# Optimization experiments

Measured on AMD Instinct MI355X. Metric: run time of the kernel, lower is better.

Reference implementation:

```python
import jax, jax.numpy as jnp
import numpy as np

BS = 8192
NUM_CLASSES = 400
D = 768


def _bilin_from_14(m14, Y, X, eH, eW):
    # Value of bilinear-resize(m14 -> (eH,eW)) at integer pixel (Y,X), computed on the fly.
    # torch F.interpolate(align_corners=False): src = (dst+0.5)*in/out - 0.5, clamped at 0.
    # m14: (bs,14,14); Y,X: (bs,14) float integer-valued coords; eH,eW: (bs,) float.
    sy = jnp.maximum((Y + 0.5) * 14.0 / eH[:, None] - 0.5, 0.0)
    sx = jnp.maximum((X + 0.5) * 14.0 / eW[:, None] - 0.5, 0.0)
    r0f = jnp.floor(sy); c0f = jnp.floor(sx)
    r0 = r0f.astype(jnp.int32); r1 = jnp.minimum(r0 + 1, 13)
    c0 = c0f.astype(jnp.int32); c1 = jnp.minimum(c0 + 1, 13)
    fy = sy - r0f; fx = sx - c0f
    b = jnp.arange(m14.shape[0])[:, None, None]
    g00 = m14[b, r0[:, :, None], c0[:, None, :]]
    g01 = m14[b, r0[:, :, None], c1[:, None, :]]
    g10 = m14[b, r1[:, :, None], c0[:, None, :]]
    g11 = m14[b, r1[:, :, None], c1[:, None, :]]
    wy = fy[:, :, None]; wx = fx[:, None, :]
    return g00 * (1 - wy) * (1 - wx) + g01 * (1 - wy) * wx + g10 * wy * (1 - wx) + g11 * wy * wx


def _get_mask(attn, o_pos, e_pos):
    # Fused, fully-batched equivalent of the per-sample python loop:
    #   resize 14x14 -> (eH,eW) bilinear; crop (top,left,oH,oW); resize -> 14x14 bilinear.
    # The final resize only reads the intermediate grid at 4 integer points per output
    # pixel, so we evaluate those points lazily via _bilin_from_14 (exact, no Emax grid).
    bs = attn.shape[0]
    m14 = attn.reshape(bs, 14, 14)
    eH = e_pos[:, 2].astype(jnp.float32); eW = e_pos[:, 3].astype(jnp.float32)
    top = (o_pos[:, 0] - e_pos[:, 0]).astype(jnp.float32)
    left = (o_pos[:, 1] - e_pos[:, 1]).astype(jnp.float32)
    oH = o_pos[:, 2].astype(jnp.float32); oW = o_pos[:, 3].astype(jnp.float32)
    i = jnp.arange(14, dtype=jnp.float32)[None, :]
    ty = jnp.maximum((i + 0.5) * oH[:, None] / 14.0 - 0.5, 0.0)  # (bs,14) coords in crop
    tx = jnp.maximum((i + 0.5) * oW[:, None] / 14.0 - 0.5, 0.0)
    y0 = jnp.floor(ty); y1 = jnp.minimum(y0 + 1.0, oH[:, None] - 1.0); wy = ty - y0
    x0 = jnp.floor(tx); x1 = jnp.minimum(x0 + 1.0, oW[:, None] - 1.0); wx = tx - x0
    Y0 = top[:, None] + y0; Y1 = top[:, None] + y1  # absolute rows in (eH,eW) grid
    X0 = left[:, None] + x0; X1 = left[:, None] + x1
    v00 = _bilin_from_14(m14, Y0, X0, eH, eW)
    v01 = _bilin_from_14(m14, Y0, X1, eH, eW)
    v10 = _bilin_from_14(m14, Y1, X0, eH, eW)
    v11 = _bilin_from_14(m14, Y1, X1, eH, eW)
    wyc = wy[:, :, None]; wxc = wx[:, None, :]
    out = v00 * (1 - wyc) * (1 - wxc) + v01 * (1 - wyc) * wxc + v10 * wyc * (1 - wxc) + v11 * wyc * wxc
    return out.reshape(bs, 196)


def _get_att_mask(attention, ratio=0.5):
    bs = attention.shape[0]
    a14 = attention.reshape(bs, 14, 14)
    # bilinear 14->7 with align_corners=False samples at frac 0.5 == 2x2 average pool
    a7 = a14.reshape(bs, 7, 2, 7, 2).mean(axis=(2, 4))
    flat = a7.reshape(bs, 49)
    n_keep = int(49 * ratio) + 1  # argsort desc, take top N+1 = 25
    _, idx = jax.lax.top_k(flat, n_keep)
    masks = jnp.ones((bs, 49), dtype=bool)
    masks = masks.at[jnp.arange(bs)[:, None], idx].set(False)
    m7 = masks.reshape(bs, 7, 7)
    full = jnp.repeat(jnp.repeat(m7, 2, axis=1), 2, axis=2)
    return full.reshape(bs, 196)


def setup_inputs() -> dict:
    key = jax.random.key(0)
    k1, k2, k3 = jax.random.split(key, 3)
    attn = jax.random.uniform(k1, (BS, 196), dtype=jnp.float32)
    rng = np.random.default_rng(0)
    IMG = 224
    eH = rng.integers(112, IMG + 1, BS); eW = rng.integers(112, IMG + 1, BS)
    eT = rng.integers(0, IMG - eH + 1); eL = rng.integers(0, IMG - eW + 1)
    def box():
        h = rng.integers(56, eH + 1); w = rng.integers(56, eW + 1)
        t = eT + rng.integers(0, eH - h + 1); l = eL + rng.integers(0, eW - w + 1)
        return np.stack([t, l, h, w], axis=1)
    e = np.stack([eT, eL, eH, eW], axis=1)
    pos = np.stack([box(), box(), e], axis=1).astype(np.int32)  # (BS,3,4)
    image_embed = jax.random.normal(k2, (2 * BS, D), dtype=jnp.float32)
    W = jax.random.normal(k3, (NUM_CLASSES, D), dtype=jnp.float32) * 0.02
    b = jnp.zeros((NUM_CLASSES,), dtype=jnp.float32)
    return {"attn": attn, "pos": jnp.asarray(pos), "image_embed": image_embed, "W": W, "b": b}


def reference(attn, pos, image_embed, W, b):
    cm1 = _get_mask(attn, pos[:, 0], pos[:, 2])
    mask1 = _get_att_mask(cm1)
    cm2 = _get_mask(attn, pos[:, 1], pos[:, 2])
    mask2 = _get_att_mask(cm2)
    mask = jnp.concatenate([mask1, mask2], axis=0)  # (2*bs,196) bool, fed to masked encoder
    logits = image_embed @ W.T + b
    return logits, mask
```

## Files before the change

kernel.cpp:

```cpp
#include <hip/hip_runtime.h>
#include <hip/hip_bf16.h>
#include <stdint.h>
#include <type_traits>

#define BSAMP 8192
#define NCLS 400
#define DIM 768
#define LOGITS_SIZE (16384LL * 400LL)
#define GEMM_BLOCKS 640
#define MASK_BLOCKS 4096
#define W_ELEMS (NCLS * DIM)

typedef __attribute__((ext_vector_type(8))) short short8;
typedef __attribute__((ext_vector_type(4))) float floatx4;

__device__ inline unsigned int packbf(float a, float b) {
    unsigned int ua = __float_as_uint(a) + 0x8000u;
    unsigned int ub = __float_as_uint(b) + 0x8000u;
    return __builtin_amdgcn_perm(ub, ua, 0x07060302u);
}

__device__ inline short8 cvt8(float4 lo, float4 hi) {
    union { unsigned int u[4]; short8 s; } r;
    r.u[0] = packbf(lo.x, lo.y);
    r.u[1] = packbf(lo.z, lo.w);
    r.u[2] = packbf(hi.x, hi.y);
    r.u[3] = packbf(hi.z, hi.w);
    return r.s;
}

__device__ inline void gload16(const void* g, void* l) {
    __builtin_amdgcn_global_load_lds((const __attribute__((address_space(1))) void*)g,
                                     (__attribute__((address_space(3))) void*)l, 16, 0, 0);
}

__global__ void cvtW_kernel(const float* __restrict__ W, unsigned short* __restrict__ ws) {
    int i = (blockIdx.x * 256 + threadIdx.x) * 4;
    if (i < W_ELEMS) {
        float4 f = *(const float4*)(W + i);
        uint2 r;
        r.x = packbf(f.x, f.y);
        r.y = packbf(f.z, f.w);
        *(uint2*)(ws + i) = r;
    }
}

__device__ inline float tap4(const float* m14, int r0, int c0, float fy, float fx) {
    int r1 = min(r0 + 1, 13);
    int c1 = min(c0 + 1, 13);
    float g00 = m14[r0 * 14 + c0];
    float g01 = m14[r0 * 14 + c1];
    float g10 = m14[r1 * 14 + c0];
    float g11 = m14[r1 * 14 + c1];
    return g00 * (1.f - fy) * (1.f - fx) + g01 * (1.f - fy) * fx +
           g10 * fy * (1.f - fx) + g11 * fy * fx;
}

struct GemmSm { unsigned short B[2][4][80 * 32]; };

template <bool USE_WS>
__global__ __launch_bounds__(256, 4) void gemm_kernel(const float* __restrict__ E,
                                                      const float* __restrict__ W,
                                                      const float* __restrict__ bias,
                                                      const unsigned short* __restrict__ wsW,
                                                      float* __restrict__ out) {
    __shared__ __align__(16) GemmSm sg;

    const int bx = blockIdx.x;
    const int t  = threadIdx.x;
    const int wv = t >> 6, ln = t & 63;

    const int xcd = bx & 7;
    const int j   = bx >> 3;
    const int n0  = (j % 5) * 80;
    const int m0  = (xcd * 16 + j / 5) * 128;
    const int quad = ln >> 4, l16 = ln & 15;

    const float* aptr0 = E + (size_t)(m0 + wv * 32 + l16) * DIM + quad * 8;
    const float* aptr1 = aptr0 + (size_t)16 * DIM;

    floatx4 acc[2][5];
#pragma unroll
    for (int g = 0; g < 2; ++g)
#pragma unroll
        for (int ni = 0; ni < 5; ++ni) acc[g][ni] = (floatx4){0.f, 0.f, 0.f, 0.f};

    if constexpr (USE_WS) {
        auto stageB = [&](int s, int buf) {
            unsigned short* dst = &sg.B[buf][wv][0];
            const int rr = ln >> 2, ch = ln & 3;
#pragma unroll
            for (int c = 0; c < 5; ++c) {
                int row = c * 16 + rr;
                const unsigned short* src = wsW + (size_t)(n0 + row) * DIM +
                                            s * 128 + wv * 32 + 8 * (ch ^ ((row >> 1) & 3));
                gload16(src, dst + c * 512);
            }
        };

        float4 pf[2][4];
        auto LD = [&](int it, int pb) {
            pf[pb][0] = *(const float4*)(aptr0 + it * 32);
            pf[pb][1] = *(const float4*)(aptr0 + it * 32 + 4);
            pf[pb][2] = *(const float4*)(aptr1 + it * 32);
            pf[pb][3] = *(const float4*)(aptr1 + it * 32 + 4);
        };

        stageB(0, 0);
        LD(0, 0);
        LD(1, 1);
        __syncthreads();

#pragma unroll
        for (int s = 0; s < 6; ++s) {
            if (s < 5) stageB(s + 1, (s + 1) & 1);
#pragma unroll
            for (int j4 = 0; j4 < 4; ++j4) {
                const int it = s * 4 + j4;
                const int pb = it & 1;
                short8 af0 = cvt8(pf[pb][0], pf[pb][1]);
                short8 af1 = cvt8(pf[pb][2], pf[pb][3]);
                if (it < 22) LD(it + 2, pb);
                const unsigned short* bb = &sg.B[s & 1][j4][0];
#pragma unroll
                for (int ni = 0; ni < 5; ++ni) {
                    int row = ni * 16 + l16;
                    short8 bfr = *(const short8*)(bb + row * 32 + 8 * (quad ^ ((row >> 1) & 3)));
                    acc[0][ni] = __builtin_amdgcn_mfma_f32_16x16x32_bf16(af0, bfr, acc[0][ni], 0, 0, 0);
                    acc[1][ni] = __builtin_amdgcn_mfma_f32_16x16x32_bf16(af1, bfr, acc[1][ni], 0, 0, 0);
                }
            }
            __syncthreads();
        }
    } else {
#pragma unroll 4
        for (int it = 0; it < 24; ++it) {
            short8 af0 = cvt8(*(const float4*)(aptr0 + it * 32), *(const float4*)(aptr0 + it * 32 + 4));
            short8 af1 = cvt8(*(const float4*)(aptr1 + it * 32), *(const float4*)(aptr1 + it * 32 + 4));
#pragma unroll
            for (int ni = 0; ni < 5; ++ni) {
                const float* wp = W + (size_t)(n0 + ni * 16 + l16) * DIM + it * 32 + quad * 8;
                short8 bfr = cvt8(*(const float4*)wp, *(const float4*)(wp + 4));
                acc[0][ni] = __builtin_amdgcn_mfma_f32_16x16x32_bf16(af0, bfr, acc[0][ni], 0, 0, 0);
                acc[1][ni] = __builtin_amdgcn_mfma_f32_16x16x32_bf16(af1, bfr, acc[1][ni], 0, 0, 0);
            }
        }
    }

    const int rowBase = m0 + wv * 32 + quad * 4;
#pragma unroll
    for (int ni = 0; ni < 5; ++ni) {
        int col = n0 + ni * 16 + l16;
        float bv = bias[col];
#pragma unroll
        for (int r = 0; r < 4; ++r) {
            out[(size_t)(rowBase + r) * NCLS + col]      = acc[0][ni][r] + bv;
            out[(size_t)(rowBase + 16 + r) * NCLS + col] = acc[1][ni][r] + bv;
        }
    }
}

struct MaskSm { float m14[4][208]; float a7[4][56]; float mv[4][56]; };

__global__ __launch_bounds__(256, 8) void mask_kernel(const float* __restrict__ attn,
                                                      const int* __restrict__ pos,
                                                      float* __restrict__ out) {
    __shared__ __align__(16) MaskSm sm;

    const int bx = blockIdx.x;
    const int t  = threadIdx.x;
    const int wv = t >> 6, ln = t & 63;

    const int p = bx * 4 + wv;
    const int b = p >> 1;
    const int o = p & 1;
    float* m14 = sm.m14[wv];

    for (int i = ln; i < 196; i += 64) m14[i] = attn[(size_t)b * 196 + i];

    const int* pb = pos + (size_t)b * 12;
    const float topf  = (float)(pb[o * 4 + 0] - pb[8]);
    const float leftf = (float)(pb[o * 4 + 1] - pb[9]);
    const float oH = (float)pb[o * 4 + 2];
    const float oW = (float)pb[o * 4 + 3];
    const float eH = (float)pb[10];
    const float eW = (float)pb[11];
    __syncthreads();

    const int i7 = ln / 7, j7 = ln - i7 * 7;
    if (ln < 49) {
        int   cI[2][2];  float cF[2][2];  float wxs[2];
        int   rI[2][2];  float rF[2][2];  float wys[2];
#pragma unroll
        for (int dx = 0; dx < 2; ++dx) {
            int ox = 2 * j7 + dx;
            float tx = fmaxf((ox + 0.5f) * oW / 14.0f - 0.5f, 0.0f);
            float x0 = floorf(tx);
            float x1 = fminf(x0 + 1.0f, oW - 1.0f);
            wxs[dx] = tx - x0;
            float X0 = leftf + x0, X1 = leftf + x1;
            float sx0 = fmaxf((X0 + 0.5f) * 14.0f / eW - 0.5f, 0.0f);
            float c0f = floorf(sx0);
            cI[dx][0] = (int)c0f; cF[dx][0] = sx0 - c0f;
            float sx1 = fmaxf((X1 + 0.5f) * 14.0f / eW - 0.5f, 0.0f);
            float c1f = floorf(sx1);
            cI[dx][1] = (int)c1f; cF[dx][1] = sx1 - c1f;
        }
#pragma unroll
        for (int dy = 0; dy < 2; ++dy) {
            int oy = 2 * i7 + dy;
            float ty = fmaxf((oy + 0.5f) * oH / 14.0f - 0.5f, 0.0f);
            float y0 = floorf(ty);
            float y1 = fminf(y0 + 1.0f, oH - 1.0f);
            wys[dy] = ty - y0;
            float Y0 = topf + y0, Y1 = topf + y1;
            float sy0 = fmaxf((Y0 + 0.5f) * 14.0f / eH - 0.5f, 0.0f);
            float r0f = floorf(sy0);
            rI[dy][0] = (int)r0f; rF[dy][0] = sy0 - r0f;
            float sy1 = fmaxf((Y1 + 0.5f) * 14.0f / eH - 0.5f, 0.0f);
            float r1f = floorf(sy1);
            rI[dy][1] = (int)r1f; rF[dy][1] = sy1 - r1f;
        }

        float s = 0.f;
#pragma unroll
        for (int dy = 0; dy < 2; ++dy) {
            float wy = wys[dy];
#pragma unroll
            for (int dx = 0; dx < 2; ++dx) {
                float wx = wxs[dx];
                float v00 = tap4(m14, rI[dy][0], cI[dx][0], rF[dy][0], cF[dx][0]);
                float v01 = tap4(m14, rI[dy][0], cI[dx][1], rF[dy][0], cF[dx][1]);
                float v10 = tap4(m14, rI[dy][1], cI[dx][0], rF[dy][1], cF[dx][0]);
                float v11 = tap4(m14, rI[dy][1], cI[dx][1], rF[dy][1], cF[dx][1]);
                float cm = v00 * (1.f - wy) * (1.f - wx) + v01 * (1.f - wy) * wx +
                           v10 * wy * (1.f - wx) + v11 * wy * wx;
                s += cm;
            }
        }
        sm.a7[wv][ln] = s * 0.25f;
    }
    __syncthreads();

    if (ln < 49) {
        float mine = sm.a7[wv][ln];
        int cnt = 0;
#pragma unroll 7
        for (int s2 = 0; s2 < 49; ++s2) {
            float v = sm.a7[wv][s2];
            cnt += (v > mine) || (v == mine && s2 < ln);
        }
        sm.mv[wv][ln] = (cnt < 25) ? 0.0f : 1.0f;
    }
    __syncthreads();

    float* ob = out + LOGITS_SIZE + (size_t)(o * BSAMP + b) * 196;
    for (int i = ln; i < 196; i += 64) {
        int oy = i / 14, ox = i - oy * 14;
        ob[i] = sm.mv[wv][(oy >> 1) * 7 + (ox >> 1)];
    }
}

extern "C" void kernel_launch(void* const* d_in, const int* in_sizes, int n_in,
                              void* d_out, int out_size, void* d_ws, size_t ws_size,
                              hipStream_t stream) {
    const float* attn = (const float*)d_in[0];
    const int*   pos  = (const int*)d_in[1];
    const float* E    = (const float*)d_in[2];
    const float* W    = (const float*)d_in[3];
    const float* bias = (const float*)d_in[4];
    float* out = (float*)d_out;

    if (ws_size >= (size_t)W_ELEMS * 2) {
        unsigned short* ws = (unsigned short*)d_ws;
        cvtW_kernel<<<300, 256, 0, stream>>>(W, ws);
        gemm_kernel<true><<<GEMM_BLOCKS, 256, 0, stream>>>(E, W, bias, ws, out);
    } else {
        gemm_kernel<false><<<GEMM_BLOCKS, 256, 0, stream>>>(E, W, bias, nullptr, out);
    }
    mask_kernel<<<MASK_BLOCKS, 256, 0, stream>>>(attn, pos, out);
}
```

Before: 166.6 us.

## Load bf16 W fragments directly from global into registers, drop LDS staging

Removes the LDS double-buffered staging of the pre-converted bf16 weight tile (global_load_lds plus barriers). Each lane now reads its B fragments straight from global memory into registers, with a 2-deep B prefetch and a 3-deep A prefetch. Launch bounds are lowered from 4 to 3 blocks per CU to make room for the extra registers. This removes LDS traffic and __syncthreads, at the cost of redundant global/L2 reads of W across waves and lower occupancy.

Result: slower. 195.8 us (+17.6%).

```diff
diff --git a/kernel.cpp b/kernel.cpp
--- a/kernel.cpp
+++ b/kernel.cpp
@@ -27,11 +27,6 @@
     r.u[2] = packbf(hi.x, hi.y);
     r.u[3] = packbf(hi.z, hi.w);
     return r.s;
-}
-
-__device__ inline void gload16(const void* g, void* l) {
-    __builtin_amdgcn_global_load_lds((const __attribute__((address_space(1))) void*)g,
-                                     (__attribute__((address_space(3))) void*)l, 16, 0, 0);
 }
 
 __global__ void cvtW_kernel(const float* __restrict__ W, unsigned short* __restrict__ ws) {
@@ -56,16 +51,12 @@
            g10 * fy * (1.f - fx) + g11 * fy * fx;
 }
 
-struct GemmSm { unsigned short B[2][4][80 * 32]; };
-
 template <bool USE_WS>
-__global__ __launch_bounds__(256, 4) void gemm_kernel(const float* __restrict__ E,
+__global__ __launch_bounds__(256, 3) void gemm_kernel(const float* __restrict__ E,
                                                       const float* __restrict__ W,
                                                       const float* __restrict__ bias,
                                                       const unsigned short* __restrict__ wsW,
                                                       float* __restrict__ out) {
-    __shared__ __align__(16) GemmSm sg;
-
     const int bx = blockIdx.x;
     const int t  = threadIdx.x;
     const int wv = t >> 6, ln = t & 63;
@@ -86,51 +77,45 @@
         for (int ni = 0; ni < 5; ++ni) acc[g][ni] = (floatx4){0.f, 0.f, 0.f, 0.f};
 
     if constexpr (USE_WS) {
-        auto stageB = [&](int s, int buf) {
-            unsigned short* dst = &sg.B[buf][wv][0];
-            const int rr = ln >> 2, ch = ln & 3;
-#pragma unroll
-            for (int c = 0; c < 5; ++c) {
-                int row = c * 16 + rr;
-                const unsigned short* src = wsW + (size_t)(n0 + row) * DIM +
-                                            s * 128 + wv * 32 + 8 * (ch ^ ((row >> 1) & 3));
-                gload16(src, dst + c * 512);
-            }
+        const unsigned short* bptr = wsW + (size_t)(n0 + l16) * DIM + quad * 8;
+
+        float4 pa[3][4];
+        short8 pb_[2][5];
+
+        auto LDA = [&](int it, int d) {
+            pa[d][0] = *(const float4*)(aptr0 + it * 32);
+            pa[d][1] = *(const float4*)(aptr0 + it * 32 + 4);
+            pa[d][2] = *(const float4*)(aptr1 + it * 32);
+            pa[d][3] = *(const float4*)(aptr1 + it * 32 + 4);
         };
-
-        float4 pf[2][4];
-        auto LD = [&](int it, int pb) {
-            pf[pb][0] = *(const float4*)(aptr0 + it * 32);
-            pf[pb][1] = *(const float4*)(aptr0 + it * 32 + 4);
-            pf[pb][2] = *(const float4*)(aptr1 + it * 32);
-            pf[pb][3] = *(const float4*)(aptr1 + it * 32 + 4);
+        auto LDB = [&](int it, int d) {
+#pragma unroll
+            for (int ni = 0; ni < 5; ++ni)
+                pb_[d][ni] = *(const short8*)(bptr + (size_t)ni * 16 * DIM + it * 32);
         };
 
-        stageB(0, 0);
-        LD(0, 0);
-        LD(1, 1);
-        __syncthreads();
-
-#pragma unroll
-        for (int s = 0; s < 6; ++s) {
-            if (s < 5) stageB(s + 1, (s + 1) & 1);
-#pragma unroll
-            for (int j4 = 0; j4 < 4; ++j4) {
-                const int it = s * 4 + j4;
-                const int pb = it & 1;
-                short8 af0 = cvt8(pf[pb][0], pf[pb][1]);
-                short8 af1 = cvt8(pf[pb][2], pf[pb][3]);
-                if (it < 22) LD(it + 2, pb);
-                const unsigned short* bb = &sg.B[s & 1][j4][0];
-#pragma unroll
-                for (int ni = 0; ni < 5; ++ni) {
-                    int row = ni * 16 + l16;
-                    short8 bfr = *(const short8*)(bb + row * 32 + 8 * (quad ^ ((row >> 1) & 3)));
-                    acc[0][ni] = __builtin_amdgcn_mfma_f32_16x16x32_bf16(af0, bfr, acc[0][ni], 0, 0, 0);
-                    acc[1][ni] = __builtin_amdgcn_mfma_f32_16x16x32_bf16(af1, bfr, acc[1][ni], 0, 0, 0);
-                }
-            }
-            __syncthreads();
+        LDA(0, 0); LDA(1, 1); LDA(2, 2);
+        LDB(0, 0); LDB(1, 1);
+
+#pragma unroll
+        for (int it = 0; it < 24; ++it) {
+            const int ia = it % 3, ib = it & 1;
+            short8 b0 = pb_[ib][0], b1 = pb_[ib][1], b2 = pb_[ib][2],
+                   b3 = pb_[ib][3], b4 = pb_[ib][4];
+            short8 af0 = cvt8(pa[ia][0], pa[ia][1]);
+            short8 af1 = cvt8(pa[ia][2], pa[ia][3]);
+            if (it < 21) LDA(it + 3, ia);
+            if (it < 22) LDB(it + 2, ib);
+            acc[0][0] = __builtin_amdgcn_mfma_f32_16x16x32_bf16(af0, b0, acc[0][0], 0, 0, 0);
+            acc[1][0] = __builtin_amdgcn_mfma_f32_16x16x32_bf16(af1, b0, acc[1][0], 0, 0, 0);
+            acc[0][1] = __builtin_amdgcn_mfma_f32_16x16x32_bf16(af0, b1, acc[0][1], 0, 0, 0);
+            acc[1][1] = __builtin_amdgcn_mfma_f32_16x16x32_bf16(af1, b1, acc[1][1], 0, 0, 0);
+            acc[0][2] = __builtin_amdgcn_mfma_f32_16x16x32_bf16(af0, b2, acc[0][2], 0, 0, 0);
+            acc[1][2] = __builtin_amdgcn_mfma_f32_16x16x32_bf16(af1, b2, acc[1][2], 0, 0, 0);
+            acc[0][3] = __builtin_amdgcn_mfma_f32_16x16x32_bf16(af0, b3, acc[0][3], 0, 0, 0);
+            acc[1][3] = __builtin_amdgcn_mfma_f32_16x16x32_bf16(af1, b3, acc[1][3], 0, 0, 0);
+            acc[0][4] = __builtin_amdgcn_mfma_f32_16x16x32_bf16(af0, b4, acc[0][4], 0, 0, 0);
+            acc[1][4] = __builtin_amdgcn_mfma_f32_16x16x32_bf16(af1, b4, acc[1][4], 0, 0, 0);
         }
     } else {
 #pragma unroll 4
```

## Halve GEMM M-tile to 64 rows and double block count

Applied to the files above, without the earlier changes.

Shrinks each GEMM block's M tile from 128 to 64 rows, so each wave computes a single 16-row MFMA group instead of two, and doubles the grid to 1280 blocks. It also adds a sched_barrier after issuing the A-prefetch so the loads are not reordered past the MFMAs. The aim is more parallelism and lower register pressure for this memory-bound fp32-input GEMM. In exchange, each staged W tile in LDS is reused across half as many rows, so W traffic and staging overhead per output roughly double.

Result: no change. 165.8 us (-0.5%).

```diff
diff --git a/kernel.cpp b/kernel.cpp
--- a/kernel.cpp
+++ b/kernel.cpp
@@ -7,7 +7,7 @@
 #define NCLS 400
 #define DIM 768
 #define LOGITS_SIZE (16384LL * 400LL)
-#define GEMM_BLOCKS 640
+#define GEMM_BLOCKS 1280
 #define MASK_BLOCKS 4096
 #define W_ELEMS (NCLS * DIM)
 
@@ -73,17 +73,14 @@
     const int xcd = bx & 7;
     const int j   = bx >> 3;
     const int n0  = (j % 5) * 80;
-    const int m0  = (xcd * 16 + j / 5) * 128;
+    const int m0  = (xcd * 32 + j / 5) * 64;
     const int quad = ln >> 4, l16 = ln & 15;
 
-    const float* aptr0 = E + (size_t)(m0 + wv * 32 + l16) * DIM + quad * 8;
-    const float* aptr1 = aptr0 + (size_t)16 * DIM;
-
-    floatx4 acc[2][5];
-#pragma unroll
-    for (int g = 0; g < 2; ++g)
-#pragma unroll
-        for (int ni = 0; ni < 5; ++ni) acc[g][ni] = (floatx4){0.f, 0.f, 0.f, 0.f};
+    const float* aptr = E + (size_t)(m0 + wv * 16 + l16) * DIM + quad * 8;
+
+    floatx4 acc[5];
+#pragma unroll
+    for (int ni = 0; ni < 5; ++ni) acc[ni] = (floatx4){0.f, 0.f, 0.f, 0.f};
 
     if constexpr (USE_WS) {
         auto stageB = [&](int s, int buf) {
@@ -98,17 +95,15 @@
             }
         };
 
-        float4 pf[2][4];
-        auto LD = [&](int it, int pb) {
-            pf[pb][0] = *(const float4*)(aptr0 + it * 32);
-            pf[pb][1] = *(const float4*)(aptr0 + it * 32 + 4);
-            pf[pb][2] = *(const float4*)(aptr1 + it * 32);
-            pf[pb][3] = *(const float4*)(aptr1 + it * 32 + 4);
+        float4 pf[2][2];
+        auto LDA = [&](int it, int d) {
+            pf[d][0] = *(const float4*)(aptr + it * 32);
+            pf[d][1] = *(const float4*)(aptr + it * 32 + 4);
         };
 
         stageB(0, 0);
-        LD(0, 0);
-        LD(1, 1);
+        LDA(0, 0);
+        LDA(1, 1);
         __syncthreads();
 
 #pragma unroll
@@ -118,16 +113,15 @@
             for (int j4 = 0; j4 < 4; ++j4) {
                 const int it = s * 4 + j4;
                 const int pb = it & 1;
-                short8 af0 = cvt8(pf[pb][0], pf[pb][1]);
-                short8 af1 = cvt8(pf[pb][2], pf[pb][3]);
-                if (it < 22) LD(it + 2, pb);
+                short8 af = cvt8(pf[pb][0], pf[pb][1]);
+                if (it < 22) LDA(it + 2, pb);
+                __builtin_amdgcn_sched_barrier(0);
                 const unsigned short* bb = &sg.B[s & 1][j4][0];
 #pragma unroll
                 for (int ni = 0; ni < 5; ++ni) {
                     int row = ni * 16 + l16;
                     short8 bfr = *(const short8*)(bb + row * 32 + 8 * (quad ^ ((row >> 1) & 3)));
-                    acc[0][ni] = __builtin_amdgcn_mfma_f32_16x16x32_bf16(af0, bfr, acc[0][ni], 0, 0, 0);
-                    acc[1][ni] = __builtin_amdgcn_mfma_f32_16x16x32_bf16(af1, bfr, acc[1][ni], 0, 0, 0);
+                    acc[ni] = __builtin_amdgcn_mfma_f32_16x16x32_bf16(af, bfr, acc[ni], 0, 0, 0);
                 }
             }
             __syncthreads();
@@ -135,27 +129,24 @@
     } else {
 #pragma unroll 4
         for (int it = 0; it < 24; ++it) {
-            short8 af0 = cvt8(*(const float4*)(aptr0 + it * 32), *(const float4*)(aptr0 + it * 32 + 4));
-            short8 af1 = cvt8(*(const float4*)(aptr1 + it * 32), *(const float4*)(aptr1 + it * 32 + 4));
+            short8 af = cvt8(*(const float4*)(aptr + it * 32), *(const float4*)(aptr + it * 32 + 4));
 #pragma unroll
             for (int ni = 0; ni < 5; ++ni) {
                 const float* wp = W + (size_t)(n0 + ni * 16 + l16) * DIM + it * 32 + quad * 8;
                 short8 bfr = cvt8(*(const float4*)wp, *(const float4*)(wp + 4));
-                acc[0][ni] = __builtin_amdgcn_mfma_f32_16x16x32_bf16(af0, bfr, acc[0][ni], 0, 0, 0);
-                acc[1][ni] = __builtin_amdgcn_mfma_f32_16x16x32_bf16(af1, bfr, acc[1][ni], 0, 0, 0);
-            }
-        }
-    }
-
-    const int rowBase = m0 + wv * 32 + quad * 4;
+                acc[ni] = __builtin_amdgcn_mfma_f32_16x16x32_bf16(af, bfr, acc[ni], 0, 0, 0);
+            }
+        }
+    }
+
+    const int rowBase = m0 + wv * 16 + quad * 4;
 #pragma unroll
     for (int ni = 0; ni < 5; ++ni) {
         int col = n0 + ni * 16 + l16;
         float bv = bias[col];
 #pragma unroll
         for (int r = 0; r < 4; ++r) {
-            out[(size_t)(rowBase + r) * NCLS + col]      = acc[0][ni][r] + bv;
-            out[(size_t)(rowBase + 16 + r) * NCLS + col] = acc[1][ni][r] + bv;
+            out[(size_t)(rowBase + r) * NCLS + col] = acc[ni][r] + bv;
         }
     }
 }
```
